# Optimization experiments

Measured on AMD Instinct MI355X. Metric: run time of the kernel, lower is better.

The kernel has to match this reference:

```python
import jax, jax.numpy as jnp
import numpy as np

B, T, C, H = 2, 1024, 768, 12
D = C // H
HID = 4 * C
EPS_YAT = 1e-6
EPS_LN = 1e-6


def yat_dense(x, kernel, bias, alpha):
    # scale = (sqrt(n_out)/log(1+n_out))**alpha
    y = x @ kernel
    dist = (jnp.sum(x * x, axis=-1, keepdims=True)
            + jnp.sum(kernel * kernel, axis=0) - 2.0 * y)
    y = (y * y) / (dist + EPS_YAT)
    if bias is not None:
        y = y + bias
    n = kernel.shape[1]
    scale = (jnp.sqrt(jnp.float32(n)) / jnp.log1p(jnp.float32(n))) ** alpha
    return y * scale


def layernorm(x, scale):
    mu = jnp.mean(x, axis=-1, keepdims=True)
    var = jnp.mean((x - mu) ** 2, axis=-1, keepdims=True)
    return (x - mu) * jax.lax.rsqrt(var + EPS_LN) * scale


def rope_table(seq_len, dim):
    freqs = jnp.exp(jnp.arange(0, dim, 2, dtype=jnp.float32)
                    * (-jnp.log(10000.0) / dim))
    angles = jnp.arange(seq_len, dtype=jnp.float32)[:, None] * freqs[None, :]
    return jnp.concatenate([jnp.cos(angles), jnp.sin(angles)], axis=-1)  # [T, D]


def block_forward(x, mask, p):
    Bc, Tc, Cc = x.shape
    h = layernorm(x, p['ln1_scale'])
    qkv = yat_dense(h, p['w_qkv'], p['b_qkv'], p['a_qkv'])  # [B,T,3C]
    qkv = qkv.reshape(Bc, Tc, 3, H, D)
    q, k, v = qkv[:, :, 0], qkv[:, :, 1], qkv[:, :, 2]      # [B,T,H,D]
    rope = rope_table(Tc, D)[:, None, :]                     # [T,1,D]
    q = q * rope
    k = k * rope
    scale = 1.0 / jnp.sqrt(jnp.float32(D))
    attn = jnp.einsum('bihd,bjhd->bhij', q, k) * scale       # [B,H,T,T]
    attn = jnp.where(mask, attn, jnp.finfo(attn.dtype).min)
    attn = jax.nn.softmax(attn, axis=-1)
    o = jnp.einsum('bhij,bjhd->bihd', attn, v).reshape(Bc, Tc, Cc)
    o = yat_dense(o, p['w_ao'], p['b_ao'], p['a_ao'])
    x = x + o
    h = layernorm(x, p['ln2_scale'])
    gate = yat_dense(h, p['w_fc'], p['b_fc'], p['a_fc'])
    u = yat_dense(h, p['w_gate'], p['b_gate'], p['a_gate'])
    u = jax.nn.gelu(u) * gate
    u = yat_dense(u, p['w_proj'], p['b_proj'], p['a_proj'])
    return x + u


def setup_inputs() -> dict:
    key = jax.random.key(0)
    ks = jax.random.split(key, 8)
    x = jax.random.normal(ks[0], (B, T, C), dtype=jnp.float32)
    mask = jnp.tril(jnp.ones((T, T), dtype=bool))[None, None]  # causal [1,1,T,T]
    w = lambda k, shp: 0.02 * jax.random.normal(k, shp, dtype=jnp.float32)
    return {
        'x': x, 'mask': mask,
        'ln1_scale': jnp.ones((C,), jnp.float32),
        'w_qkv': w(ks[1], (C, 3 * C)), 'b_qkv': jnp.zeros((3 * C,), jnp.float32),
        'a_qkv': jnp.ones((1,), jnp.float32),
        'w_ao': w(ks[2], (C, C)), 'b_ao': jnp.zeros((C,), jnp.float32),
        'a_ao': jnp.ones((1,), jnp.float32),
        'ln2_scale': jnp.ones((C,), jnp.float32),
        'w_fc': w(ks[3], (C, HID)), 'b_fc': jnp.zeros((HID,), jnp.float32),
        'a_fc': jnp.ones((1,), jnp.float32),
        'w_gate': w(ks[4], (C, HID)), 'b_gate': jnp.zeros((HID,), jnp.float32),
        'a_gate': jnp.ones((1,), jnp.float32),
        'w_proj': w(ks[5], (HID, C)), 'b_proj': jnp.zeros((C,), jnp.float32),
        'a_proj': jnp.ones((1,), jnp.float32),
    }


def reference(x, mask, ln1_scale, w_qkv, b_qkv, a_qkv, w_ao, b_ao, a_ao,
              ln2_scale, w_fc, b_fc, a_fc, w_gate, b_gate, a_gate,
              w_proj, b_proj, a_proj):
    p = dict(ln1_scale=ln1_scale, w_qkv=w_qkv, b_qkv=b_qkv, a_qkv=a_qkv,
             w_ao=w_ao, b_ao=b_ao, a_ao=a_ao, ln2_scale=ln2_scale,
             w_fc=w_fc, b_fc=b_fc, a_fc=a_fc, w_gate=w_gate, b_gate=b_gate,
             a_gate=a_gate, w_proj=w_proj, b_proj=b_proj, a_proj=a_proj)
    return block_forward(x, mask, p)
```

## Files before the change

kernel.cpp:

```cpp
#include <hip/hip_runtime.h>
#include <cstdint>

#define DEVFN static __device__ __forceinline__

typedef __bf16 bf16x8 __attribute__((ext_vector_type(8)));
typedef float f32x4 __attribute__((ext_vector_type(4)));
typedef unsigned short us4 __attribute__((ext_vector_type(4)));

DEVFN unsigned short f2bf(float f) {
  unsigned u = __float_as_uint(f);
  u += 0x7fffu + ((u >> 16) & 1u);
  return (unsigned short)(u >> 16);
}
DEVFN float bf2f(unsigned short h) { return __uint_as_float(((unsigned)h) << 16); }
DEVFN void async16(const void* g, void* l) {
  __builtin_amdgcn_global_load_lds((__attribute__((address_space(1))) const void*)g,
                                   (__attribute__((address_space(3))) void*)l, 16, 0, 0);
}
DEVFN float gelu_t(float u) {
  return 0.5f * u * (1.f + tanhf(0.7978845608028654f * (u + 0.044715f * u * u * u)));
}

__global__ __launch_bounds__(256) void k_rope(float* __restrict__ rope) {
  int g = blockIdx.x * 256 + threadIdx.x;
  int t = g >> 6, dd = g & 63, i = dd & 31;
  float fr = __expf(-0.2878231366242558f * (float)i);
  float ang = (float)t * fr;
  rope[g] = (dd < 32) ? cosf(ang) : sinf(ang);
}

__global__ __launch_bounds__(256) void k_transpose(const float* __restrict__ W,
    unsigned short* __restrict__ Wt, float* __restrict__ cn, int N, int K) {
  __shared__ float tile[32][33];
  __shared__ float part[8][32];
  int tx = threadIdx.x & 31, ty = threadIdx.x >> 5;
  int tn = blockIdx.x, tk = blockIdx.y;
  float acc = 0.f;
  #pragma unroll
  for (int j = 0; j < 4; ++j) {
    int r = ty + j * 8;
    float v = W[(long)(tk * 32 + r) * N + tn * 32 + tx];
    tile[r][tx] = v;
    acc += v * v;
  }
  part[ty][tx] = acc;
  __syncthreads();
  #pragma unroll
  for (int j = 0; j < 4; ++j) {
    int rr = ty + j * 8;
    Wt[(long)(tn * 32 + rr) * K + tk * 32 + tx] = f2bf(tile[tx][rr]);
  }
  if (ty == 0) {
    float s = part[0][tx];
    #pragma unroll
    for (int jj = 1; jj < 8; ++jj) s += part[jj][tx];
    atomicAdd(&cn[tn * 32 + tx], s);
  }
}

__global__ __launch_bounds__(256) void k_ln(const float* __restrict__ x,
    const float* __restrict__ g, unsigned short* __restrict__ h, float* __restrict__ row2) {
  int row = blockIdx.x, tid = threadIdx.x;
  const float* xr = x + (long)row * 768;
  float v0 = xr[tid], v1 = xr[tid + 256], v2 = xr[tid + 512];
  float s = v0 + v1 + v2;
  float ss = v0 * v0 + v1 * v1 + v2 * v2;
  #pragma unroll
  for (int o = 32; o; o >>= 1) { s += __shfl_xor(s, o); ss += __shfl_xor(ss, o); }
  __shared__ float red[12];
  int wv = tid >> 6;
  if ((tid & 63) == 0) { red[wv] = s; red[wv + 4] = ss; }
  __syncthreads();
  s = red[0] + red[1] + red[2] + red[3];
  ss = red[4] + red[5] + red[6] + red[7];
  float mu = s * (1.f / 768.f);
  float var = ss * (1.f / 768.f) - mu * mu;
  float rs = rsqrtf(var + 1e-6f);
  float h0 = (v0 - mu) * rs * g[tid];
  float h1 = (v1 - mu) * rs * g[tid + 256];
  float h2 = (v2 - mu) * rs * g[tid + 512];
  unsigned short* hr = h + (long)row * 768;
  hr[tid] = f2bf(h0); hr[tid + 256] = f2bf(h1); hr[tid + 512] = f2bf(h2);
  float p = h0 * h0 + h1 * h1 + h2 * h2;
  #pragma unroll
  for (int o = 32; o; o >>= 1) p += __shfl_xor(p, o);
  if ((tid & 63) == 0) red[8 + wv] = p;
  __syncthreads();
  if (tid == 0) row2[row] = red[8] + red[9] + red[10] + red[11];
}

constexpr int M_QKV = 0, M_AO = 1, M_PART = 2;

struct GemmArgs {
  const unsigned short* A; const unsigned short* Bt;
  const float* arow2; const float* wcol2; const float* bias; const float* alpha;
  int N; int ks;
  const float* rope;
  unsigned short* qo; unsigned short* ko; unsigned short* vo;
  const float* xf; float* xo;
  float* part;
};

template <int MODE, int NI>
__global__ __launch_bounds__(256, 4) void k_gemm(GemmArgs p) {
  __shared__ __align__(16) unsigned short As[3][2048];
  __shared__ __align__(16) unsigned short Bs[3][4096];
  const int tid = threadIdx.x, wave = tid >> 6, lane = tid & 63;
  const int quad = lane >> 4, l = lane & 15;
  const int bm = blockIdx.x * 64, bn = blockIdx.y * 128;
  const int kb = (MODE == M_PART) ? (int)blockIdx.z * (NI * 32) : 0;
  const int ks = p.ks;
  const int wm = (wave & 1) * 32, wn = (wave >> 1) * 64;
  const f32x4 fzero = {0.f, 0.f, 0.f, 0.f};
  f32x4 acc[2][4];
  #pragma unroll
  for (int i = 0; i < 2; ++i)
    #pragma unroll
    for (int j = 0; j < 4; ++j) acc[i][j] = fzero;
  const int sw = (l >> 1) & 3;

  auto stage = [&](int s, int k0) {
    {
      int ci = tid;
      int r = ci >> 2;
      int c = (ci & 3) ^ ((r >> 1) & 3);
      async16(p.A + (long)(bm + r) * ks + kb + k0 + c * 8, &As[s][ci * 8]);
    }
    #pragma unroll
    for (int it = 0; it < 2; ++it) {
      int ci = tid + it * 256;
      int r = ci >> 2;
      int c = (ci & 3) ^ ((r >> 1) & 3);
      async16(p.Bt + (long)(bn + r) * ks + kb + k0 + c * 8, &Bs[s][ci * 8]);
    }
  };
  auto compute = [&](int s) {
    bf16x8 af[2], bfv[4];
    #pragma unroll
    for (int mi = 0; mi < 2; ++mi)
      af[mi] = *(const bf16x8*)&As[s][(wm + mi * 16 + l) * 32 + ((quad ^ sw) * 8)];
    #pragma unroll
    for (int ni = 0; ni < 4; ++ni)
      bfv[ni] = *(const bf16x8*)&Bs[s][(wn + ni * 16 + l) * 32 + ((quad ^ sw) * 8)];
    #pragma unroll
    for (int mi = 0; mi < 2; ++mi)
      #pragma unroll
      for (int ni = 0; ni < 4; ++ni)
        acc[mi][ni] = __builtin_amdgcn_mfma_f32_16x16x32_bf16(af[mi], bfv[ni], acc[mi][ni], 0, 0, 0);
  };
  auto iter = [&](int s, int i) {
    if (i + 1 >= NI) { asm volatile("s_waitcnt vmcnt(0)" ::: "memory"); }
    else             { asm volatile("s_waitcnt vmcnt(3)" ::: "memory"); }
    __builtin_amdgcn_s_barrier();
    asm volatile("" ::: "memory");
    if (i + 2 < NI) stage(s == 0 ? 2 : s - 1, (i + 2) * 32);
    compute(s);
  };

  stage(0, 0);
  stage(1, 32);
  int i = 0;
  while (i < NI) {
    iter(0, i); ++i;
    iter(1, i); ++i;
    iter(2, i); ++i;
  }

  if constexpr (MODE == M_PART) {
    float* slab = p.part + (long)blockIdx.z * (2048 * 768);
    #pragma unroll
    for (int ni = 0; ni < 4; ++ni) {
      const int j = bn + wn + ni * 16 + l;
      #pragma unroll
      for (int mi = 0; mi < 2; ++mi) {
        const int i0 = bm + wm + mi * 16 + quad * 4;
        #pragma unroll
        for (int rg = 0; rg < 4; ++rg)
          slab[(long)(i0 + rg) * 768 + j] = acc[mi][ni][rg];
      }
    }
  } else {
    const float al = p.alpha[0];
    const float nn = (float)p.N;
    const float ys = powf(sqrtf(nn) / log1pf(nn), al);
    #pragma unroll
    for (int ni = 0; ni < 4; ++ni) {
      const int j = bn + wn + ni * 16 + l;
      const float w2 = p.wcol2[j];
      const float bj = p.bias[j];
      int s3 = 0, hh = 0, dd = 0;
      if constexpr (MODE == M_QKV) { s3 = j / 768; int rem = j - s3 * 768; hh = rem >> 6; dd = rem & 63; }
      #pragma unroll
      for (int mi = 0; mi < 2; ++mi) {
        const int i0 = bm + wm + mi * 16 + quad * 4;
        float vv[4];
        #pragma unroll
        for (int rg = 0; rg < 4; ++rg) {
          const float y = acc[mi][ni][rg];
          const float dist = p.arow2[i0 + rg] + w2 - 2.f * y + 1e-6f;
          vv[rg] = (y * y / dist + bj) * ys;
        }
        if constexpr (MODE == M_QKV) {
          int b = i0 >> 10, t0 = i0 & 1023;
          if (s3 == 2) {
            us4 pk = {f2bf(vv[0]), f2bf(vv[1]), f2bf(vv[2]), f2bf(vv[3])};
            *(us4*)&p.vo[((long)(b * 12 + hh) * 64 + dd) * 1024 + t0] = pk;
          } else {
            unsigned short* dst = (s3 == 0) ? p.qo : p.ko;
            #pragma unroll
            for (int rg = 0; rg < 4; ++rg) {
              float ro = p.rope[(t0 + rg) * 64 + dd];
              dst[((long)(b * 12 + hh) * 1024 + t0 + rg) * 64 + dd] = f2bf(vv[rg] * ro);
            }
          }
        } else {
          #pragma unroll
          for (int rg = 0; rg < 4; ++rg) {
            long idx = (long)(i0 + rg) * 768 + j;
            p.xo[idx] = p.xf[idx] + vv[rg];
          }
        }
      }
    }
  }
}

struct EpiArgs {
  const float* slab; const float* arow2; const float* wcol2;
  const float* bias; const float* alpha; const float* xo; float* outf;
};
__global__ __launch_bounds__(256) void k_proj_epi(EpiArgs p) {
  int g = blockIdx.x * 256 + threadIdx.x;
  int i = g / 192, jv = (g - i * 192) * 4;
  long base = (long)i * 768 + jv;
  f32x4 y = *(const f32x4*)(p.slab + base);
  y += *(const f32x4*)(p.slab + 1572864 + base);
  y += *(const f32x4*)(p.slab + 2 * 1572864 + base);
  y += *(const f32x4*)(p.slab + 3 * 1572864 + base);
  const float a2 = p.arow2[i];
  const float ys = powf(sqrtf(768.f) / log1pf(768.f), p.alpha[0]);
  f32x4 xo4 = *(const f32x4*)(p.xo + base);
  f32x4 out;
  #pragma unroll
  for (int c = 0; c < 4; ++c) {
    float yy = y[c];
    float dist = a2 + p.wcol2[jv + c] - 2.f * yy + 1e-6f;
    out[c] = xo4[c] + (yy * yy / dist + p.bias[jv + c]) * ys;
  }
  *(f32x4*)(p.outf + base) = out;
}

struct MlpArgs {
  const unsigned short* A; const unsigned short* Bf; const unsigned short* Bg;
  const float* arow2; const float* w2f; const float* w2g;
  const float* bf; const float* bg; const float* af_; const float* ag_;
  unsigned short* mlp; float* mrow2;
};

__global__ __launch_bounds__(256, 2) void k_mlp(MlpArgs p) {
  constexpr int NI = 24, K = 768;
  __shared__ __align__(16) unsigned short As[3][2048];
  __shared__ __align__(16) unsigned short Bfs[3][4096];
  __shared__ __align__(16) unsigned short Bgs[3][4096];
  const int tid = threadIdx.x, wave = tid >> 6, lane = tid & 63;
  const int quad = lane >> 4, l = lane & 15;
  const int bm = blockIdx.x * 64, bn = blockIdx.y * 128;
  const int wm = (wave & 1) * 32, wn = (wave >> 1) * 64;
  const f32x4 fzero = {0.f, 0.f, 0.f, 0.f};
  f32x4 accf[2][4], accg[2][4];
  #pragma unroll
  for (int i = 0; i < 2; ++i)
    #pragma unroll
    for (int j = 0; j < 4; ++j) { accf[i][j] = fzero; accg[i][j] = fzero; }
  const int sw = (l >> 1) & 3;

  auto stage = [&](int s, int k0) {
    {
      int ci = tid;
      int r = ci >> 2;
      int c = (ci & 3) ^ ((r >> 1) & 3);
      async16(p.A + (long)(bm + r) * K + k0 + c * 8, &As[s][ci * 8]);
    }
    #pragma unroll
    for (int it = 0; it < 2; ++it) {
      int ci = tid + it * 256;
      int r = ci >> 2;
      int c = (ci & 3) ^ ((r >> 1) & 3);
      async16(p.Bf + (long)(bn + r) * K + k0 + c * 8, &Bfs[s][ci * 8]);
      async16(p.Bg + (long)(bn + r) * K + k0 + c * 8, &Bgs[s][ci * 8]);
    }
  };
  auto compute = [&](int s) {
    bf16x8 af[2], bff[4], bfg[4];
    #pragma unroll
    for (int mi = 0; mi < 2; ++mi)
      af[mi] = *(const bf16x8*)&As[s][(wm + mi * 16 + l) * 32 + ((quad ^ sw) * 8)];
    #pragma unroll
    for (int ni = 0; ni < 4; ++ni) {
      bff[ni] = *(const bf16x8*)&Bfs[s][(wn + ni * 16 + l) * 32 + ((quad ^ sw) * 8)];
      bfg[ni] = *(const bf16x8*)&Bgs[s][(wn + ni * 16 + l) * 32 + ((quad ^ sw) * 8)];
    }
    #pragma unroll
    for (int mi = 0; mi < 2; ++mi)
      #pragma unroll
      for (int ni = 0; ni < 4; ++ni) {
        accf[mi][ni] = __builtin_amdgcn_mfma_f32_16x16x32_bf16(af[mi], bff[ni], accf[mi][ni], 0, 0, 0);
        accg[mi][ni] = __builtin_amdgcn_mfma_f32_16x16x32_bf16(af[mi], bfg[ni], accg[mi][ni], 0, 0, 0);
      }
  };
  auto iter = [&](int s, int i) {
    if (i + 1 >= NI) { asm volatile("s_waitcnt vmcnt(0)" ::: "memory"); }
    else             { asm volatile("s_waitcnt vmcnt(5)" ::: "memory"); }
    __builtin_amdgcn_s_barrier();
    asm volatile("" ::: "memory");
    if (i + 2 < NI) stage(s == 0 ? 2 : s - 1, (i + 2) * 32);
    compute(s);
  };

  stage(0, 0);
  stage(1, 32);
  int i = 0;
  while (i < NI) {
    iter(0, i); ++i;
    iter(1, i); ++i;
    iter(2, i); ++i;
  }

  const float ysf = powf(sqrtf(3072.f) / log1pf(3072.f), p.af_[0]);
  const float ysg = powf(sqrtf(3072.f) / log1pf(3072.f), p.ag_[0]);
  float w2f[4], w2g[4], bjf[4], bjg[4]; int js[4];
  #pragma unroll
  for (int ni = 0; ni < 4; ++ni) {
    int j = bn + wn + ni * 16 + l;
    js[ni] = j; w2f[ni] = p.w2f[j]; w2g[ni] = p.w2g[j]; bjf[ni] = p.bf[j]; bjg[ni] = p.bg[j];
  }
  #pragma unroll
  for (int mi = 0; mi < 2; ++mi) {
    #pragma unroll
    for (int rg = 0; rg < 4; ++rg) {
      const int ii = bm + wm + mi * 16 + quad * 4 + rg;
      const float a2 = p.arow2[ii];
      float rsum = 0.f;
      #pragma unroll
      for (int ni = 0; ni < 4; ++ni) {
        float yf = accf[mi][ni][rg];
        float gate = (yf * yf / (a2 + w2f[ni] - 2.f * yf + 1e-6f) + bjf[ni]) * ysf;
        float yg = accg[mi][ni][rg];
        float u  = (yg * yg / (a2 + w2g[ni] - 2.f * yg + 1e-6f) + bjg[ni]) * ysg;
        float out = gelu_t(u) * gate;
        p.mlp[(long)ii * 3072 + js[ni]] = f2bf(out);
        rsum += out * out;
      }
      #pragma unroll
      for (int o = 8; o; o >>= 1) rsum += __shfl_xor(rsum, o);
      if (l == 0) atomicAdd(&p.mrow2[ii], rsum);
    }
  }
}

__global__ __launch_bounds__(256) void k_attn(const unsigned short* __restrict__ qb,
    const unsigned short* __restrict__ kb, const unsigned short* __restrict__ vb,
    unsigned short* __restrict__ ob, float* __restrict__ orow2) {
  __shared__ __align__(16) unsigned short Qs[64 * 64];
  __shared__ __align__(16) unsigned short Ks[64 * 64];
  __shared__ __align__(16) unsigned short Vs[64 * 64];
  __shared__ __align__(16) unsigned short Ps[4 * 16 * 64];
  const int tid = threadIdx.x, wave = tid >> 6, lane = tid & 63;
  const int quad = lane >> 4, l = lane & 15;
  const int qt = blockIdx.x, bh = blockIdx.y;
  const int b = bh / 12, hh = bh % 12;
  const int q0 = qt * 64;
  const f32x4 fzero = {0.f, 0.f, 0.f, 0.f};

  const unsigned short* qg = qb + ((long)bh * 1024 + q0) * 64;
  #pragma unroll
  for (int it = 0; it < 2; ++it) {
    int ci = tid + it * 256;
    int r = ci >> 3;
    int c = (ci & 7) ^ (r & 7);
    async16(qg + (long)r * 64 + c * 8, &Qs[ci * 8]);
  }
  __builtin_amdgcn_s_waitcnt(0);
  __syncthreads();
  bf16x8 aq[2];
  #pragma unroll
  for (int ks = 0; ks < 2; ++ks)
    aq[ks] = *(const bf16x8*)&Qs[(wave * 16 + l) * 64 + (((ks * 4 + quad) ^ (l & 7)) * 8)];

  f32x4 O[4];
  float mi_[4], li[4];
  #pragma unroll
  for (int f = 0; f < 4; ++f) O[f] = fzero;
  #pragma unroll
  for (int r = 0; r < 4; ++r) { mi_[r] = -1e30f; li[r] = 0.f; }

  for (int jt = 0; jt <= qt; ++jt) {
    __syncthreads();
    const unsigned short* kg = kb + ((long)bh * 1024 + jt * 64) * 64;
    const unsigned short* vg = vb + (long)bh * 64 * 1024 + jt * 64;
    #pragma unroll
    for (int it = 0; it < 2; ++it) {
      int ci = tid + it * 256;
      int r = ci >> 3;
      int c = (ci & 7) ^ (r & 7);
      async16(kg + (long)r * 64 + c * 8, &Ks[ci * 8]);
      async16(vg + (long)r * 1024 + c * 8, &Vs[ci * 8]);
    }
    __builtin_amdgcn_s_waitcnt(0);
    __syncthreads();

    f32x4 S[4];
    #pragma unroll
    for (int f = 0; f < 4; ++f) S[f] = fzero;
    #pragma unroll
    for (int ks = 0; ks < 2; ++ks) {
      #pragma unroll
      for (int f = 0; f < 4; ++f) {
        bf16x8 bk = *(const bf16x8*)&Ks[(f * 16 + l) * 64 + (((ks * 4 + quad) ^ (l & 7)) * 8)];
        S[f] = __builtin_amdgcn_mfma_f32_16x16x32_bf16(aq[ks], bk, S[f], 0, 0, 0);
      }
    }
    const bool diag = (jt == qt);
    #pragma unroll
    for (int f = 0; f < 4; ++f)
      #pragma unroll
      for (int r = 0; r < 4; ++r) {
        float v = S[f][r] * 0.125f;
        if (diag && (f * 16 + l > wave * 16 + quad * 4 + r)) v = -1e30f;
        S[f][r] = v;
      }
    #pragma unroll
    for (int r = 0; r < 4; ++r) {
      float mx = fmaxf(fmaxf(S[0][r], S[1][r]), fmaxf(S[2][r], S[3][r]));
      #pragma unroll
      for (int o = 8; o; o >>= 1) mx = fmaxf(mx, __shfl_xor(mx, o));
      float mnew = fmaxf(mi_[r], mx);
      float alr = __expf(mi_[r] - mnew);
      float sum = 0.f;
      #pragma unroll
      for (int f = 0; f < 4; ++f) {
        float e = __expf(S[f][r] - mnew);
        S[f][r] = e;
        sum += e;
      }
      #pragma unroll
      for (int o = 8; o; o >>= 1) sum += __shfl_xor(sum, o);
      li[r] = li[r] * alr + sum;
      #pragma unroll
      for (int f = 0; f < 4; ++f) O[f][r] *= alr;
      mi_[r] = mnew;
    }
    #pragma unroll
    for (int f = 0; f < 4; ++f)
      #pragma unroll
      for (int r = 0; r < 4; ++r) {
        int i = quad * 4 + r;
        int j = f * 16 + l;
        int pch = (j >> 3) ^ (i & 7);
        Ps[wave * 1024 + i * 64 + pch * 8 + (j & 7)] = f2bf(S[f][r]);
      }
    #pragma unroll
    for (int ks = 0; ks < 2; ++ks) {
      bf16x8 ap = *(const bf16x8*)&Ps[wave * 1024 + l * 64 + (((ks * 4 + quad) ^ (l & 7)) * 8)];
      #pragma unroll
      for (int f = 0; f < 4; ++f) {
        bf16x8 bv = *(const bf16x8*)&Vs[(f * 16 + l) * 64 + (((ks * 4 + quad) ^ (l & 7)) * 8)];
        O[f] = __builtin_amdgcn_mfma_f32_16x16x32_bf16(ap, bv, O[f], 0, 0, 0);
      }
    }
  }
  #pragma unroll
  for (int f = 0; f < 4; ++f)
    #pragma unroll
    for (int r = 0; r < 4; ++r) {
      int t = q0 + wave * 16 + quad * 4 + r;
      int dd = f * 16 + l;
      float v = O[f][r] / li[r];
      ob[((long)(b * 1024 + t) * 12 + hh) * 64 + dd] = f2bf(v);
    }
  #pragma unroll
  for (int r = 0; r < 4; ++r) {
    float rsum = 0.f;
    #pragma unroll
    for (int f = 0; f < 4; ++f) { float v = O[f][r] / li[r]; rsum += v * v; }
    #pragma unroll
    for (int o = 8; o; o >>= 1) rsum += __shfl_xor(rsum, o);
    if (l == 0) {
      int t = q0 + wave * 16 + quad * 4 + r;
      atomicAdd(&orow2[b * 1024 + t], rsum);
    }
  }
}

extern "C" void kernel_launch(void* const* d_in, const int* in_sizes, int n_in,
                              void* d_out, int out_size, void* d_ws, size_t ws_size,
                              hipStream_t stream) {
  (void)in_sizes; (void)n_in; (void)out_size;
  char* w = (char*)d_ws;
  size_t off = 0;
  auto alloc = [&](size_t bytes) -> void* {
    void* p = w + off;
    off = (off + bytes + 255) & ~(size_t)255;
    return p;
  };
  float* rope            = (float*)alloc(65536 * 4);
  unsigned short* wtqkv  = (unsigned short*)alloc((size_t)2304 * 768 * 2);
  unsigned short* wtao   = (unsigned short*)alloc((size_t)768 * 768 * 2);
  unsigned short* wtfc   = (unsigned short*)alloc((size_t)3072 * 768 * 2);
  unsigned short* wtgate = (unsigned short*)alloc((size_t)3072 * 768 * 2);
  unsigned short* wtproj = (unsigned short*)alloc((size_t)768 * 3072 * 2);
  float* zeroed          = (float*)alloc(14080 * 4);
  unsigned short* h1     = (unsigned short*)alloc((size_t)2048 * 768 * 2);
  float* hrow1           = (float*)alloc(2048 * 4);
  unsigned short* qbuf   = (unsigned short*)alloc((size_t)2048 * 768 * 2);
  unsigned short* kbuf   = (unsigned short*)alloc((size_t)2048 * 768 * 2);
  unsigned short* vbuf   = (unsigned short*)alloc((size_t)2048 * 768 * 2);
  unsigned short* obuf   = (unsigned short*)alloc((size_t)2048 * 768 * 2);
  float* xo              = (float*)alloc((size_t)2048 * 768 * 4);
  unsigned short* h2     = (unsigned short*)alloc((size_t)2048 * 768 * 2);
  float* hrow2           = (float*)alloc(2048 * 4);
  unsigned short* mlp    = (unsigned short*)alloc((size_t)2048 * 3072 * 2);
  float* slabs           = (float*)alloc((size_t)4 * 2048 * 768 * 4);
  if (off > ws_size) return;

  float* wcol2  = zeroed;
  float* orow2  = zeroed + 9984;
  float* mrow2  = zeroed + 9984 + 2048;
  float* c_qkv  = wcol2 + 0;
  float* c_ao   = wcol2 + 2304;
  float* c_fc   = wcol2 + 3072;
  float* c_gate = wcol2 + 6144;
  float* c_proj = wcol2 + 9216;

  const float* xin = (const float*)d_in[0];

  hipMemsetAsync(zeroed, 0, 14080 * 4, stream);
  k_rope<<<256, 256, 0, stream>>>(rope);

  k_transpose<<<dim3(72, 24), 256, 0, stream>>>((const float*)d_in[3],  wtqkv,  c_qkv,  2304, 768);
  k_transpose<<<dim3(24, 24), 256, 0, stream>>>((const float*)d_in[6],  wtao,   c_ao,   768,  768);
  k_transpose<<<dim3(96, 24), 256, 0, stream>>>((const float*)d_in[10], wtfc,   c_fc,   3072, 768);
  k_transpose<<<dim3(96, 24), 256, 0, stream>>>((const float*)d_in[13], wtgate, c_gate, 3072, 768);
  k_transpose<<<dim3(24, 96), 256, 0, stream>>>((const float*)d_in[16], wtproj, c_proj, 768,  3072);

  k_ln<<<2048, 256, 0, stream>>>(xin, (const float*)d_in[2], h1, hrow1);

  GemmArgs gq = {};
  gq.A = h1; gq.Bt = wtqkv; gq.arow2 = hrow1; gq.wcol2 = c_qkv;
  gq.bias = (const float*)d_in[4]; gq.alpha = (const float*)d_in[5];
  gq.N = 2304; gq.ks = 768;
  gq.rope = rope; gq.qo = qbuf; gq.ko = kbuf; gq.vo = vbuf;
  k_gemm<M_QKV, 24><<<dim3(32, 18), 256, 0, stream>>>(gq);

  k_attn<<<dim3(16, 24), 256, 0, stream>>>(qbuf, kbuf, vbuf, obuf, orow2);

  GemmArgs ga = {};
  ga.A = obuf; ga.Bt = wtao; ga.arow2 = orow2; ga.wcol2 = c_ao;
  ga.bias = (const float*)d_in[7]; ga.alpha = (const float*)d_in[8];
  ga.N = 768; ga.ks = 768;
  ga.xf = xin; ga.xo = xo;
  k_gemm<M_AO, 24><<<dim3(32, 6), 256, 0, stream>>>(ga);

  k_ln<<<2048, 256, 0, stream>>>(xo, (const float*)d_in[9], h2, hrow2);

  MlpArgs gm = {};
  gm.A = h2; gm.Bf = wtfc; gm.Bg = wtgate; gm.arow2 = hrow2;
  gm.w2f = c_fc; gm.w2g = c_gate;
  gm.bf = (const float*)d_in[11]; gm.bg = (const float*)d_in[14];
  gm.af_ = (const float*)d_in[12]; gm.ag_ = (const float*)d_in[15];
  gm.mlp = mlp; gm.mrow2 = mrow2;
  k_mlp<<<dim3(32, 24), 256, 0, stream>>>(gm);

  GemmArgs gp = {};
  gp.A = mlp; gp.Bt = wtproj;
  gp.N = 768; gp.ks = 3072;
  gp.part = slabs;
  k_gemm<M_PART, 24><<<dim3(32, 6, 4), 256, 0, stream>>>(gp);

  EpiArgs ge = {};
  ge.slab = slabs; ge.arow2 = mrow2; ge.wcol2 = c_proj;
  ge.bias = (const float*)d_in[17]; ge.alpha = (const float*)d_in[18];
  ge.xo = xo; ge.outf = (float*)d_out;
  k_proj_epi<<<1536, 256, 0, stream>>>(ge);
}
```

Measured before the change: 311.4 us.

## Add XCD-aware block swizzle, merge transposes, enlarge MLP tile, halve proj split-K

Adds an XCD-aware block index swizzle to the GEMM, attention and MLP kernels so that neighbouring tiles land on the same chiplet's L2. It also merges the five weight-transpose launches into one launch driven by an offset table. The fused MLP kernel moves to a 128x128 tile with a two-stage pipeline instead of three stages, which raises operand reuse but doubles accumulator registers. The projection GEMM goes from four K splits to two, halving the slab traffic its epilogue reads back. The risks are register pressure and lower occupancy in the MLP kernel, and fewer blocks in the projection GEMM.

```diff
diff --git a/kernel.cpp b/kernel.cpp
--- a/kernel.cpp
+++ b/kernel.cpp
@@ -19,6 +19,9 @@
 }
 DEVFN float gelu_t(float u) {
   return 0.5f * u * (1.f + tanhf(0.7978845608028654f * (u + 0.044715f * u * u * u)));
+}
+DEVFN int xcd_swizzle(int lin, int total) {
+  return (lin & 7) * (total >> 3) + (lin >> 3);
 }
 
 __global__ __launch_bounds__(256) void k_rope(float* __restrict__ rope) {
@@ -29,12 +32,25 @@
   rope[g] = (dd < 32) ? cosf(ang) : sinf(ang);
 }
 
-__global__ __launch_bounds__(256) void k_transpose(const float* __restrict__ W,
-    unsigned short* __restrict__ Wt, float* __restrict__ cn, int N, int K) {
+struct TrArgs {
+  const float* W[5]; unsigned short* Wt[5]; float* cn[5];
+  int N[5]; int off[6];
+};
+__global__ __launch_bounds__(256) void k_transpose(TrArgs a) {
   __shared__ float tile[32][33];
   __shared__ float part[8][32];
+  int lin = blockIdx.x;
+  int e = 0;
+  while (lin >= a.off[e + 1]) ++e;
+  int local = lin - a.off[e];
+  const int N = a.N[e];
+  int nbx = N >> 5;
+  int tn = local % nbx, tk = local / nbx;
+  const float* W = a.W[e];
+  unsigned short* Wt = a.Wt[e];
+  float* cn = a.cn[e];
+  const int K = (e == 4) ? 3072 : 768;
   int tx = threadIdx.x & 31, ty = threadIdx.x >> 5;
-  int tn = blockIdx.x, tk = blockIdx.y;
   float acc = 0.f;
   #pragma unroll
   for (int j = 0; j < 4; ++j) {
@@ -101,14 +117,19 @@
   float* part;
 };
 
-template <int MODE, int NI>
+template <int MODE, int NI, int NBM, int NBN, int NZ>
 __global__ __launch_bounds__(256, 4) void k_gemm(GemmArgs p) {
   __shared__ __align__(16) unsigned short As[3][2048];
   __shared__ __align__(16) unsigned short Bs[3][4096];
   const int tid = threadIdx.x, wave = tid >> 6, lane = tid & 63;
   const int quad = lane >> 4, l = lane & 15;
-  const int bm = blockIdx.x * 64, bn = blockIdx.y * 128;
-  const int kb = (MODE == M_PART) ? (int)blockIdx.z * (NI * 32) : 0;
+  constexpr int TOTAL = NBM * NBN * NZ;
+  const int g = xcd_swizzle(blockIdx.x, TOTAL);
+  const int bm = (g % NBM) * 64;
+  const int rest = g / NBM;
+  const int bn = (rest % NBN) * 128;
+  const int z = rest / NBN;
+  const int kb = z * (NI * 32);
   const int ks = p.ks;
   const int wm = (wave & 1) * 32, wn = (wave >> 1) * 64;
   const f32x4 fzero = {0.f, 0.f, 0.f, 0.f};
@@ -167,7 +188,7 @@
   }
 
   if constexpr (MODE == M_PART) {
-    float* slab = p.part + (long)blockIdx.z * (2048 * 768);
+    float* slab = p.part + (long)z * (2048 * 768);
     #pragma unroll
     for (int ni = 0; ni < 4; ++ni) {
       const int j = bn + wn + ni * 16 + l;
@@ -235,8 +256,6 @@
   long base = (long)i * 768 + jv;
   f32x4 y = *(const f32x4*)(p.slab + base);
   y += *(const f32x4*)(p.slab + 1572864 + base);
-  y += *(const f32x4*)(p.slab + 2 * 1572864 + base);
-  y += *(const f32x4*)(p.slab + 3 * 1572864 + base);
   const float a2 = p.arow2[i];
   const float ys = powf(sqrtf(768.f) / log1pf(768.f), p.alpha[0]);
   f32x4 xo4 = *(const f32x4*)(p.xo + base);
@@ -259,41 +278,44 @@
 
 __global__ __launch_bounds__(256, 2) void k_mlp(MlpArgs p) {
   constexpr int NI = 24, K = 768;
-  __shared__ __align__(16) unsigned short As[3][2048];
-  __shared__ __align__(16) unsigned short Bfs[3][4096];
-  __shared__ __align__(16) unsigned short Bgs[3][4096];
+  __shared__ __align__(16) unsigned short As[2][4096];
+  __shared__ __align__(16) unsigned short Bfs[2][4096];
+  __shared__ __align__(16) unsigned short Bgs[2][4096];
   const int tid = threadIdx.x, wave = tid >> 6, lane = tid & 63;
   const int quad = lane >> 4, l = lane & 15;
-  const int bm = blockIdx.x * 64, bn = blockIdx.y * 128;
-  const int wm = (wave & 1) * 32, wn = (wave >> 1) * 64;
+  const int g = xcd_swizzle(blockIdx.x, 16 * 24);
+  const int bm = (g % 16) * 128, bn = (g / 16) * 128;
+  const int wm = (wave & 1) * 64, wn = (wave >> 1) * 64;
   const f32x4 fzero = {0.f, 0.f, 0.f, 0.f};
-  f32x4 accf[2][4], accg[2][4];
-  #pragma unroll
-  for (int i = 0; i < 2; ++i)
+  f32x4 accf[4][4], accg[4][4];
+  #pragma unroll
+  for (int i = 0; i < 4; ++i)
     #pragma unroll
     for (int j = 0; j < 4; ++j) { accf[i][j] = fzero; accg[i][j] = fzero; }
   const int sw = (l >> 1) & 3;
 
   auto stage = [&](int s, int k0) {
-    {
-      int ci = tid;
-      int r = ci >> 2;
-      int c = (ci & 3) ^ ((r >> 1) & 3);
-      async16(p.A + (long)(bm + r) * K + k0 + c * 8, &As[s][ci * 8]);
-    }
     #pragma unroll
     for (int it = 0; it < 2; ++it) {
       int ci = tid + it * 256;
       int r = ci >> 2;
       int c = (ci & 3) ^ ((r >> 1) & 3);
+      async16(p.A  + (long)(bm + r) * K + k0 + c * 8, &As[s][ci * 8]);
       async16(p.Bf + (long)(bn + r) * K + k0 + c * 8, &Bfs[s][ci * 8]);
       async16(p.Bg + (long)(bn + r) * K + k0 + c * 8, &Bgs[s][ci * 8]);
     }
   };
-  auto compute = [&](int s) {
-    bf16x8 af[2], bff[4], bfg[4];
-    #pragma unroll
-    for (int mi = 0; mi < 2; ++mi)
+
+  stage(0, 0);
+  for (int i = 0; i < NI; ++i) {
+    int s = i & 1;
+    asm volatile("s_waitcnt vmcnt(0)" ::: "memory");
+    __builtin_amdgcn_s_barrier();
+    asm volatile("" ::: "memory");
+    if (i + 1 < NI) stage(s ^ 1, (i + 1) * 32);
+    bf16x8 af[4], bff[4], bfg[4];
+    #pragma unroll
+    for (int mi = 0; mi < 4; ++mi)
       af[mi] = *(const bf16x8*)&As[s][(wm + mi * 16 + l) * 32 + ((quad ^ sw) * 8)];
     #pragma unroll
     for (int ni = 0; ni < 4; ++ni) {
@@ -301,29 +323,12 @@
       bfg[ni] = *(const bf16x8*)&Bgs[s][(wn + ni * 16 + l) * 32 + ((quad ^ sw) * 8)];
     }
     #pragma unroll
-    for (int mi = 0; mi < 2; ++mi)
+    for (int mi = 0; mi < 4; ++mi)
       #pragma unroll
       for (int ni = 0; ni < 4; ++ni) {
         accf[mi][ni] = __builtin_amdgcn_mfma_f32_16x16x32_bf16(af[mi], bff[ni], accf[mi][ni], 0, 0, 0);
         accg[mi][ni] = __builtin_amdgcn_mfma_f32_16x16x32_bf16(af[mi], bfg[ni], accg[mi][ni], 0, 0, 0);
       }
-  };
-  auto iter = [&](int s, int i) {
-    if (i + 1 >= NI) { asm volatile("s_waitcnt vmcnt(0)" ::: "memory"); }
-    else             { asm volatile("s_waitcnt vmcnt(5)" ::: "memory"); }
-    __builtin_amdgcn_s_barrier();
-    asm volatile("" ::: "memory");
-    if (i + 2 < NI) stage(s == 0 ? 2 : s - 1, (i + 2) * 32);
-    compute(s);
-  };
-
-  stage(0, 0);
-  stage(1, 32);
-  int i = 0;
-  while (i < NI) {
-    iter(0, i); ++i;
-    iter(1, i); ++i;
-    iter(2, i); ++i;
   }
 
   const float ysf = powf(sqrtf(3072.f) / log1pf(3072.f), p.af_[0]);
@@ -335,7 +340,7 @@
     js[ni] = j; w2f[ni] = p.w2f[j]; w2g[ni] = p.w2g[j]; bjf[ni] = p.bf[j]; bjg[ni] = p.bg[j];
   }
   #pragma unroll
-  for (int mi = 0; mi < 2; ++mi) {
+  for (int mi = 0; mi < 4; ++mi) {
     #pragma unroll
     for (int rg = 0; rg < 4; ++rg) {
       const int ii = bm + wm + mi * 16 + quad * 4 + rg;
@@ -367,7 +372,8 @@
   __shared__ __align__(16) unsigned short Ps[4 * 16 * 64];
   const int tid = threadIdx.x, wave = tid >> 6, lane = tid & 63;
   const int quad = lane >> 4, l = lane & 15;
-  const int qt = blockIdx.x, bh = blockIdx.y;
+  const int g = xcd_swizzle(blockIdx.x, 16 * 24);
+  const int qt = g % 16, bh = g / 16;
   const int b = bh / 12, hh = bh % 12;
   const int q0 = qt * 64;
   const f32x4 fzero = {0.f, 0.f, 0.f, 0.f};
@@ -520,7 +526,7 @@
   unsigned short* h2     = (unsigned short*)alloc((size_t)2048 * 768 * 2);
   float* hrow2           = (float*)alloc(2048 * 4);
   unsigned short* mlp    = (unsigned short*)alloc((size_t)2048 * 3072 * 2);
-  float* slabs           = (float*)alloc((size_t)4 * 2048 * 768 * 4);
+  float* slabs           = (float*)alloc((size_t)2 * 2048 * 768 * 4);
   if (off > ws_size) return;
 
   float* wcol2  = zeroed;
@@ -537,11 +543,15 @@
   hipMemsetAsync(zeroed, 0, 14080 * 4, stream);
   k_rope<<<256, 256, 0, stream>>>(rope);
 
-  k_transpose<<<dim3(72, 24), 256, 0, stream>>>((const float*)d_in[3],  wtqkv,  c_qkv,  2304, 768);
-  k_transpose<<<dim3(24, 24), 256, 0, stream>>>((const float*)d_in[6],  wtao,   c_ao,   768,  768);
-  k_transpose<<<dim3(96, 24), 256, 0, stream>>>((const float*)d_in[10], wtfc,   c_fc,   3072, 768);
-  k_transpose<<<dim3(96, 24), 256, 0, stream>>>((const float*)d_in[13], wtgate, c_gate, 3072, 768);
-  k_transpose<<<dim3(24, 96), 256, 0, stream>>>((const float*)d_in[16], wtproj, c_proj, 768,  3072);
+  TrArgs ta;
+  ta.W[0] = (const float*)d_in[3];  ta.Wt[0] = wtqkv;  ta.cn[0] = c_qkv;  ta.N[0] = 2304;
+  ta.W[1] = (const float*)d_in[6];  ta.Wt[1] = wtao;   ta.cn[1] = c_ao;   ta.N[1] = 768;
+  ta.W[2] = (const float*)d_in[10]; ta.Wt[2] = wtfc;   ta.cn[2] = c_fc;   ta.N[2] = 3072;
+  ta.W[3] = (const float*)d_in[13]; ta.Wt[3] = wtgate; ta.cn[3] = c_gate; ta.N[3] = 3072;
+  ta.W[4] = (const float*)d_in[16]; ta.Wt[4] = wtproj; ta.cn[4] = c_proj; ta.N[4] = 768;
+  ta.off[0] = 0; ta.off[1] = 1728; ta.off[2] = 2304; ta.off[3] = 4608;
+  ta.off[4] = 6912; ta.off[5] = 9216;
+  k_transpose<<<9216, 256, 0, stream>>>(ta);
 
   k_ln<<<2048, 256, 0, stream>>>(xin, (const float*)d_in[2], h1, hrow1);
 
@@ -550,16 +560,16 @@
   gq.bias = (const float*)d_in[4]; gq.alpha = (const float*)d_in[5];
   gq.N = 2304; gq.ks = 768;
   gq.rope = rope; gq.qo = qbuf; gq.ko = kbuf; gq.vo = vbuf;
-  k_gemm<M_QKV, 24><<<dim3(32, 18), 256, 0, stream>>>(gq);
-
-  k_attn<<<dim3(16, 24), 256, 0, stream>>>(qbuf, kbuf, vbuf, obuf, orow2);
+  k_gemm<M_QKV, 24, 32, 18, 1><<<576, 256, 0, stream>>>(gq);
+
+  k_attn<<<384, 256, 0, stream>>>(qbuf, kbuf, vbuf, obuf, orow2);
 
   GemmArgs ga = {};
   ga.A = obuf; ga.Bt = wtao; ga.arow2 = orow2; ga.wcol2 = c_ao;
   ga.bias = (const float*)d_in[7]; ga.alpha = (const float*)d_in[8];
   ga.N = 768; ga.ks = 768;
   ga.xf = xin; ga.xo = xo;
-  k_gemm<M_AO, 24><<<dim3(32, 6), 256, 0, stream>>>(ga);
+  k_gemm<M_AO, 24, 32, 6, 1><<<192, 256, 0, stream>>>(ga);
 
   k_ln<<<2048, 256, 0, stream>>>(xo, (const float*)d_in[9], h2, hrow2);
 
@@ -569,13 +579,13 @@
   gm.bf = (const float*)d_in[11]; gm.bg = (const float*)d_in[14];
   gm.af_ = (const float*)d_in[12]; gm.ag_ = (const float*)d_in[15];
   gm.mlp = mlp; gm.mrow2 = mrow2;
-  k_mlp<<<dim3(32, 24), 256, 0, stream>>>(gm);
+  k_mlp<<<384, 256, 0, stream>>>(gm);
 
   GemmArgs gp = {};
   gp.A = mlp; gp.Bt = wtproj;
   gp.N = 768; gp.ks = 3072;
   gp.part = slabs;
-  k_gemm<M_PART, 24><<<dim3(32, 6, 4), 256, 0, stream>>>(gp);
+  k_gemm<M_PART, 48, 32, 6, 2><<<384, 256, 0, stream>>>(gp);
 
   EpiArgs ge = {};
   ge.slab = slabs; ge.arow2 = mrow2; ge.wcol2 = c_proj;
```

Measured after the change: 290.8 us. 1.07x faster.
